# Performance work log

Measured on AMD Instinct MI355X. Metric: run time of the kernel, lower is better.

## Reference

```python
import jax, jax.numpy as jnp
import numpy as np
import math

NLAT, NLON, LMAX, MMAX = 128, 256, 50, 50
K = 3  # three_nn

# ---- precompute: Clenshaw-Curtis quadrature (torch_harmonics 'equiangular') ----
def _cc_nodes_weights(n):
    Nn = n - 1
    theta = np.pi * np.arange(n) / Nn
    v = np.zeros(n)
    for k in range(1, Nn // 2 + 1):
        b = 1.0 if 2 * k == Nn else 2.0
        v += b * np.cos(2 * k * theta) / (4 * k * k - 1)
    w = (2.0 / Nn) * (1.0 - v)
    w[0] *= 0.5
    w[-1] *= 0.5
    return np.cos(theta), w

# ---- precompute: orthonormal associated Legendre P_l^m(cos theta), csphase ----
def _legpoly(lmax, mmax, cost):
    sint = np.sqrt(np.clip(1.0 - cost ** 2, 0.0, None))
    p = np.zeros((mmax, lmax, cost.shape[0]))
    pmm = np.full(cost.shape[0], np.sqrt(1.0 / (4.0 * np.pi)))
    for m in range(mmax):
        if m > 0:
            pmm = -pmm * np.sqrt((2.0 * m + 1.0) / (2.0 * m)) * sint
        p[m, m] = pmm
        if m + 1 < lmax:
            p[m, m + 1] = np.sqrt(2.0 * m + 3.0) * cost * pmm
        for l in range(m + 2, lmax):
            a = np.sqrt((4.0 * l * l - 1.0) / (l * l - m * m))
            b = np.sqrt(((2.0 * l + 1.0) * (l - 1 + m) * (l - 1 - m)) / ((2.0 * l - 3.0) * (l * l - m * m)))
            p[m, l] = a * cost * p[m, l - 1] - b * p[m, l - 2]
    return p

_cost, _w = _cc_nodes_weights(NLAT)
_PCTW = jnp.asarray((_legpoly(LMAX, MMAX, _cost) * _w[None, None, :]).astype(np.float32))  # (mmax,lmax,nlat)

_gx, _gy = np.meshgrid(np.arange(NLAT), np.arange(-NLAT, NLAT), indexing='ij')
_GRID = jnp.asarray((np.stack([_gx.ravel(), _gy.ravel()], -1) / NLAT * np.pi).astype(np.float32))  # (M,2)

_RECTW = jnp.asarray(np.exp(-(LMAX - np.arange(1, LMAX + 1)) ** 2 / (2.0 * LMAX ** 2)).astype(np.float32))  # (lmax,)


def to_spherical(coords):
    # coords: (B,N,3) -> r:(B,N), sph:(B,N,2) = [arccos(x/r), azimuth in [0,2pi)]
    sq = coords ** 2
    pn = jnp.sqrt(jnp.flip(jnp.cumsum(jnp.flip(sq, -1), -1), -1))  # pn[...,i] = ||coords[...,i:]||
    r = pn[..., 0]
    phi = jnp.arccos(coords[..., :-2] / pn[..., :-2])
    a = jnp.arccos(coords[..., -2] / pn[..., -2])
    phi_final = a + (2.0 * math.pi - 2.0 * a) * (coords[..., -1] < 0)
    return r, jnp.concatenate([phi, phi_final[..., None]], axis=-1)


def interp_to_grid(coords):
    # spherical transform + 3-NN (squared dists) + distance-weighted interpolation onto the lat/lon grid
    r, sph = to_spherical(coords)
    sph = sph.at[..., 1].add(-math.pi)
    # brute-force pairwise squared distances grid(M,2) vs sph(B,N,2): (B,M,N)
    d2 = (jnp.sum(_GRID ** 2, -1)[None, :, None] + jnp.sum(sph ** 2, -1)[:, None, :]
          - 2.0 * jnp.einsum('md,bnd->bmn', _GRID, sph))
    _, idx = jax.lax.top_k(-jax.lax.stop_gradient(d2), K)  # (B,M,K), ascending distance
    sel = jax.vmap(lambda s, i: s[i])(sph, idx)            # (B,M,K,2)
    fsel = jax.vmap(lambda f, i: f[i])(r, idx)             # (B,M,K)
    dk = jnp.sum((_GRID[None, :, None, :] - sel) ** 2, -1)  # recompute selected sq-dists (differentiable)
    w = dk / jnp.sum(dk, -1, keepdims=True)                # weights = dist / sum(dist), as in source
    return jnp.sum(fsel * w, -1).reshape(-1, NLAT, NLON)


def sht_real(x):
    # RealSHT (equiangular, ortho): rfft(norm='forward')*2pi, then Legendre*quadrature einsum; real part only
    xf = jnp.fft.rfft(x, axis=-1)[..., :MMAX] * (2.0 * math.pi / NLON)
    return jnp.einsum('bkm,mlk->blm', jnp.real(xf).astype(jnp.float32), _PCTW)  # (B,lmax,mmax)


def setup_inputs() -> dict:
    key = jax.random.key(0)
    k1, k2 = jax.random.split(key)
    pred = jax.random.normal(k1, (2, 2048, 3), dtype=jnp.float32)
    target = jax.random.normal(k2, (2, 2048, 3), dtype=jnp.float32)
    return {"pred": pred, "target": target}


def reference(pred, target):
    pc = sht_real(interp_to_grid(pred))
    tc = sht_real(interp_to_grid(target))
    return jnp.mean(jnp.sum((pc - tc) ** 2 * _RECTW[None, :, None], axis=(1, 2)))
```

## Files before the change

kernel.cpp:

```cpp
#include <hip/hip_runtime.h>
#include <math.h>

#define PI_D 3.14159265358979323846
#define PIF  3.14159265358979323846f
#define NLAT 128
#define NLON 256
#define LMAX 50
#define MMAX 50
#define NPTS 2048
#define NBT 16
#define NBA 32
#define NBIN (NBT * NBA)
#define WBIN 0.19634954084936207f
#define INVW 5.092958178940651f
#define BIG 1e30f
#define KMASK 0xFFFFF800u

__device__ __forceinline__ void insert3(float kf, float& k0, float& k1, float& k2) {
    float n1 = __builtin_amdgcn_fmed3f(kf, k0, k1);
    float n2 = __builtin_amdgcn_fmed3f(kf, k1, k2);
    k0 = fminf(kf, k0);
    k1 = n1;
    k2 = n2;
}

__device__ __forceinline__ float mkkey(float gt, float gl, float2 tl, int idx) {
    float dt = gt - tl.x, dl = gl - tl.y;
    float d = fmaf(dt, dt, dl * dl);
    return __uint_as_float((__float_as_uint(d) & KMASK) | (unsigned)idx);
}

__global__ __launch_bounds__(256) void prep_kernel(
    const float* __restrict__ pred, const float* __restrict__ tgt,
    float2* __restrict__ gbtl, float* __restrict__ gbr, int* __restrict__ goff,
    float* __restrict__ pctwT, float* __restrict__ out) {

    __shared__ float2 s_btl[NPTS];
    __shared__ float  s_br[NPTS];
    __shared__ int    s_cnt[NBIN];
    __shared__ int    s_off[NBIN + 1];

    int bid = blockIdx.x;
    int t = threadIdx.x;

    if (bid >= 4) {
        int k = bid - 4;
        int m = t;
        if (k == 0 && m == 0) out[0] = 0.0f;
        if (m >= MMAX) return;

        double thd = PI_D * (double)k / 127.0;
        float cost = (float)cos(thd);
        float sint = (float)sin(thd);

        float c2 = (float)cos(2.0 * thd);
        float two_c2 = 2.0f * c2;
        float cp = 1.0f, cc = c2, v = 0.0f;
        for (int tt = 1; tt <= 63; ++tt) {
            v += 2.0f * cc / (float)(4 * tt * tt - 1);
            float cn = two_c2 * cc - cp;
            cp = cc;
            cc = cn;
        }
        float w = (2.0f / 127.0f) * (1.0f - v);
        if (k == 0 || k == 127) w *= 0.5f;

        float pmm = sqrtf(1.0f / (4.0f * PIF));
        for (int i = 1; i <= m; ++i)
            pmm = -pmm * sqrtf((2.0f * (float)i + 1.0f) / (2.0f * (float)i)) * sint;

        float* o = pctwT + (size_t)k * MMAX + m;
        for (int l = 0; l < m; ++l) o[(size_t)l * NLAT * MMAX] = 0.0f;
        o[(size_t)m * NLAT * MMAX] = pmm * w;
        float plm2 = pmm, plm1 = 0.0f;
        if (m + 1 < LMAX) {
            plm1 = sqrtf(2.0f * (float)m + 3.0f) * cost * pmm;
            o[(size_t)(m + 1) * NLAT * MMAX] = plm1 * w;
        }
        for (int l = m + 2; l < LMAX; ++l) {
            float fl = (float)l;
            float denom = fl * fl - (float)(m * m);
            float a = sqrtf((4.0f * fl * fl - 1.0f) / denom);
            float b = sqrtf(((2.0f * fl + 1.0f) * (float)(l - 1 + m) * (float)(l - 1 - m)) /
                            ((2.0f * fl - 3.0f) * denom));
            float p = a * cost * plm1 - b * plm2;
            o[(size_t)l * NLAT * MMAX] = p * w;
            plm2 = plm1;
            plm1 = p;
        }
        return;
    }

    int f = bid;
    const float* src = ((f < 2) ? pred : tgt) + (size_t)(f & 1) * NPTS * 3;

    s_cnt[t] = 0;
    s_cnt[t + 256] = 0;
    __syncthreads();

    float pth[8], paz[8], pr[8];
    int pbin[8];
#pragma unroll
    for (int i = 0; i < 8; ++i) {
        int n = t + 256 * i;
        float x = src[3 * n], y = src[3 * n + 1], z = src[3 * n + 2];
        float s1 = z * z;
        float s2 = s1 + y * y;
        float s3 = s2 + x * x;
        float r = sqrtf(s3);
        float rho = sqrtf(s2);
        float th = acosf(x / r);
        float a = acosf(y / rho);
        float az = (z < 0.0f) ? (a + (2.0f * PIF - 2.0f * a)) : a;
        az -= PIF;
        int bt = min(max((int)(th * INVW), 0), NBT - 1);
        int ba = min(max((int)((az + PIF) * INVW), 0), NBA - 1);
        int b = bt * NBA + ba;
        pth[i] = th; paz[i] = az; pr[i] = r; pbin[i] = b;
        atomicAdd(&s_cnt[b], 1);
    }
    __syncthreads();

    if (t == 0) s_off[NBIN] = NPTS;
    if (t < 64) {
        int base = t * 8;
        int loc[8];
        int run = 0;
#pragma unroll
        for (int i = 0; i < 8; ++i) { loc[i] = run; run += s_cnt[base + i]; }
        int x = run;
#pragma unroll
        for (int d = 1; d < 64; d <<= 1) {
            int y = __shfl_up(x, d);
            if (t >= d) x += y;
        }
        int ex = x - run;
#pragma unroll
        for (int i = 0; i < 8; ++i) s_off[base + i] = ex + loc[i];
    }
    __syncthreads();
    s_cnt[t] = s_off[t];
    s_cnt[t + 256] = s_off[t + 256];
    __syncthreads();
#pragma unroll
    for (int i = 0; i < 8; ++i) {
        int pos = atomicAdd(&s_cnt[pbin[i]], 1);
        s_btl[pos] = make_float2(pth[i], paz[i]);
        s_br[pos] = pr[i];
    }
    __syncthreads();

    for (int n = t; n < NPTS; n += 256) {
        gbtl[(size_t)f * NPTS + n] = s_btl[n];
        gbr[(size_t)f * NPTS + n] = s_br[n];
    }
    for (int n = t; n <= NBIN; n += 256) goff[f * (NBIN + 1) + n] = s_off[n];
}

__global__ __launch_bounds__(256) void knn_kernel(
    const float2* __restrict__ gbtl, const float* __restrict__ gbr,
    const int* __restrict__ goff, float* __restrict__ fre) {

    __shared__ float2 s_btl[NPTS];
    __shared__ float  s_br[NPTS];
    __shared__ int    s_off[NBIN + 1];
    __shared__ float  ctab[NLON];
    __shared__ float  row[NLON];
    __shared__ float  part[200];

    int bid = blockIdx.x;
    int t = threadIdx.x;
    int f = bid >> 7;
    int lat = bid & 127;

    {
        const float4* b4 = (const float4*)(gbtl + (size_t)f * NPTS);
        float4* s4 = (float4*)s_btl;
        for (int i = t; i < NPTS / 2; i += 256) s4[i] = b4[i];
        const float4* r4 = (const float4*)(gbr + (size_t)f * NPTS);
        float4* sr4 = (float4*)s_br;
        for (int i = t; i < NPTS / 4; i += 256) sr4[i] = r4[i];
        const int* go = goff + f * (NBIN + 1);
        for (int i = t; i <= NBIN; i += 256) s_off[i] = go[i];
        ctab[t] = (float)cos(2.0 * PI_D * (double)t / (double)NLON);
    }
    __syncthreads();

    int j = t;
    float gt = (float)((double)lat * PI_D / 128.0);
    float gl = (float)(((double)j - 128.0) * PI_D / 128.0);
    float glp = gl + PIF;
    int bt0 = lat >> 3;
    int ba0 = j >> 3;

    auto scan_seg = [&](int i, int i1, float& q0, float& q1, float& q2) {
        for (; i + 4 <= i1; i += 4) {
            float2 a0 = s_btl[i];
            float2 a1 = s_btl[i + 1];
            float2 a2 = s_btl[i + 2];
            float2 a3 = s_btl[i + 3];
            insert3(mkkey(gt, gl, a0, i), q0, q1, q2);
            insert3(mkkey(gt, gl, a1, i + 1), q0, q1, q2);
            insert3(mkkey(gt, gl, a2, i + 2), q0, q1, q2);
            insert3(mkkey(gt, gl, a3, i + 3), q0, q1, q2);
        }
        for (; i < i1; ++i)
            insert3(mkkey(gt, gl, s_btl[i], i), q0, q1, q2);
    };

    float k0 = BIG, k1 = BIG, k2 = BIG;
    {
        int rtl = max(bt0 - 1, 0), rth = min(bt0 + 1, NBT - 1);
        int bal = max(ba0 - 1, 0), bah = min(ba0 + 1, NBA - 1);
        for (int bt = rtl; bt <= rth; ++bt)
            scan_seg(s_off[bt * NBA + bal], s_off[bt * NBA + bah + 1], k0, k1, k2);
    }

    bool done;
    {
        float safe = BIG;
        if (bt0 - 1 > 0)       safe = fminf(safe, gt - (float)(bt0 - 1) * WBIN);
        if (bt0 + 1 < NBT - 1) safe = fminf(safe, (float)(bt0 + 2) * WBIN - gt);
        if (ba0 - 1 > 0)       safe = fminf(safe, glp - (float)(ba0 - 1) * WBIN);
        if (ba0 + 1 < NBA - 1) safe = fminf(safe, (float)(ba0 + 2) * WBIN - glp);
        done = (k2 <= safe * safe);
    }

    for (int R = 2; R <= 31; ++R) {
        if (__all(done)) break;
        if (!done) {
            int btl = bt0 - R, bth = bt0 + R;
            int lo = max(btl, 0), hi = min(bth, NBT - 1);
            int bal = max(ba0 - R, 0), bah = min(ba0 + R, NBA - 1);
            for (int bt = lo; bt <= hi; ++bt) {
                if (bt == btl || bt == bth) {
                    scan_seg(s_off[bt * NBA + bal], s_off[bt * NBA + bah + 1], k0, k1, k2);
                } else {
                    if (ba0 - R >= 0) {
                        int b = bt * NBA + ba0 - R;
                        scan_seg(s_off[b], s_off[b + 1], k0, k1, k2);
                    }
                    if (ba0 + R <= NBA - 1) {
                        int b = bt * NBA + ba0 + R;
                        scan_seg(s_off[b], s_off[b + 1], k0, k1, k2);
                    }
                }
            }
            float safe = BIG;
            if (bt0 - R > 0)       safe = fminf(safe, gt - (float)(bt0 - R) * WBIN);
            if (bt0 + R < NBT - 1) safe = fminf(safe, (float)(bt0 + R + 1) * WBIN - gt);
            if (ba0 - R > 0)       safe = fminf(safe, glp - (float)(ba0 - R) * WBIN);
            if (ba0 + R < NBA - 1) safe = fminf(safe, (float)(ba0 + R + 1) * WBIN - glp);
            if (k2 <= safe * safe) done = true;
        }
    }

    {
        int i0 = __float_as_uint(k0) & 0x7FF;
        int i1 = __float_as_uint(k1) & 0x7FF;
        int i2 = __float_as_uint(k2) & 0x7FF;
        float2 p0 = s_btl[i0];
        float2 p1 = s_btl[i1];
        float2 p2 = s_btl[i2];
        float dt0 = gt - p0.x, dl0 = gl - p0.y;
        float dt1 = gt - p1.x, dl1 = gl - p1.y;
        float dt2 = gt - p2.x, dl2 = gl - p2.y;
        float d0 = fmaf(dt0, dt0, dl0 * dl0);
        float d1 = fmaf(dt1, dt1, dl1 * dl1);
        float d2 = fmaf(dt2, dt2, dl2 * dl2);
        float s = d0 + d1 + d2;
        row[j] = (d0 * s_br[i0] + d1 * s_br[i1] + d2 * s_br[i2]) / s;
    }
    __syncthreads();

    if (t < 200) {
        int mm = t >> 2, q = t & 3;
        int bs = q * 64;
        float a0 = 0.0f, a1 = 0.0f, a2 = 0.0f, a3 = 0.0f;
        int p = (bs * mm) & (NLON - 1);
        int st1 = mm & (NLON - 1);
        int st2 = (2 * mm) & (NLON - 1);
        int st3 = (3 * mm) & (NLON - 1);
        int st4 = (4 * mm) & (NLON - 1);
        for (int i = 0; i < 64; i += 4) {
            a0 += row[bs + i] * ctab[p];
            a1 += row[bs + i + 1] * ctab[(p + st1) & (NLON - 1)];
            a2 += row[bs + i + 2] * ctab[(p + st2) & (NLON - 1)];
            a3 += row[bs + i + 3] * ctab[(p + st3) & (NLON - 1)];
            p = (p + st4) & (NLON - 1);
        }
        part[t] = (a0 + a1) + (a2 + a3);
    }
    __syncthreads();
    if (t < MMAX) {
        const float* pp = part + t * 4;
        fre[(f * NLAT + lat) * MMAX + t] =
            ((pp[0] + pp[1]) + (pp[2] + pp[3])) * (float)(2.0 * PI_D / (double)NLON);
    }
}

__global__ __launch_bounds__(256) void contract_loss(const float* __restrict__ fre,
                                                     const float* __restrict__ pctwT,
                                                     float* __restrict__ out) {
    int b = blockIdx.x / LMAX;
    int l = blockIdx.x % LMAX;
    int mm = threadIdx.x & 63;
    int kq = threadIdx.x >> 6;
    __shared__ float sp[4][64], st_[4][64];
    float pc = 0.0f, tc = 0.0f;
    if (mm < MMAX) {
        const float* pw = pctwT + ((size_t)l * NLAT + kq * 32) * MMAX + mm;
        const float* fp = fre + ((size_t)b * NLAT + kq * 32) * MMAX + mm;
        const float* ft = fre + ((size_t)(2 + b) * NLAT + kq * 32) * MMAX + mm;
#pragma unroll 8
        for (int k = 0; k < 32; ++k) {
            float w = pw[k * MMAX];
            pc += fp[k * MMAX] * w;
            tc += ft[k * MMAX] * w;
        }
    }
    sp[kq][mm] = pc;
    st_[kq][mm] = tc;
    __syncthreads();
    if (threadIdx.x < 64) {
        int m2 = threadIdx.x;
        float pcs = (sp[0][m2] + sp[1][m2]) + (sp[2][m2] + sp[3][m2]);
        float tcs = (st_[0][m2] + st_[1][m2]) + (st_[2][m2] + st_[3][m2]);
        float diff = pcs - tcs;
        double dl_ = (double)(49 - l);
        float rw = (float)exp(-(dl_ * dl_) / 5000.0);
        float contrib = (m2 < MMAX) ? diff * diff * rw * 0.5f : 0.0f;
        for (int off = 32; off > 0; off >>= 1) contrib += __shfl_down(contrib, off);
        if (m2 == 0) atomicAdd(out, contrib);
    }
}

extern "C" void kernel_launch(void* const* d_in, const int* in_sizes, int n_in,
                              void* d_out, int out_size, void* d_ws, size_t ws_size,
                              hipStream_t stream) {
    const float* pred = (const float*)d_in[0];
    const float* tgt = (const float*)d_in[1];
    float* ws = (float*)d_ws;

    float*  pctwT = ws;
    float*  fre   = ws + 320000;
    float2* gbtl  = (float2*)(ws + 345600);
    float*  gbr   = ws + 345600 + 16384;
    int*    goff  = (int*)(ws + 345600 + 16384 + 8192);
    float* out = (float*)d_out;

    prep_kernel<<<132, 256, 0, stream>>>(pred, tgt, gbtl, gbr, goff, pctwT, out);
    knn_kernel<<<512, 256, 0, stream>>>(gbtl, gbr, goff, fre);
    contract_loss<<<2 * LMAX, 256, 0, stream>>>(fre, pctwT, out);
}
```

Baseline: 91.29 us.

## Fuse prep and kNN kernels, recomputing binned point sort per block

Merges the point-preparation kernel into the kNN/DFT kernel: each of the 512 latitude blocks now converts coordinates to spherical form and bin-sorts all 2048 points itself in shared memory, instead of reading results written to global memory by a separate launch. This removes one kernel launch, the global round-trip, and the dependency between the two kernels. In exchange the spherical conversion and counting sort are repeated 128 times per field. The DFT partial sums are also re-indexed so threads are grouped by quarter rather than interleaved.

```diff
diff --git a/kernel.cpp b/kernel.cpp
--- a/kernel.cpp
+++ b/kernel.cpp
@@ -30,21 +30,23 @@
     return __uint_as_float((__float_as_uint(d) & KMASK) | (unsigned)idx);
 }
 
-__global__ __launch_bounds__(256) void prep_kernel(
+__global__ __launch_bounds__(256) void fused_main(
     const float* __restrict__ pred, const float* __restrict__ tgt,
-    float2* __restrict__ gbtl, float* __restrict__ gbr, int* __restrict__ goff,
-    float* __restrict__ pctwT, float* __restrict__ out) {
+    float* __restrict__ pctwT, float* __restrict__ fre, float* __restrict__ out) {
 
     __shared__ float2 s_btl[NPTS];
     __shared__ float  s_br[NPTS];
     __shared__ int    s_cnt[NBIN];
     __shared__ int    s_off[NBIN + 1];
+    __shared__ float  ctab[NLON];
+    __shared__ float  row[NLON];
+    __shared__ float  part[256];
 
     int bid = blockIdx.x;
     int t = threadIdx.x;
 
-    if (bid >= 4) {
-        int k = bid - 4;
+    if (bid >= 512) {
+        int k = bid - 512;
         int m = t;
         if (k == 0 && m == 0) out[0] = 0.0f;
         if (m >= MMAX) return;
@@ -91,11 +93,13 @@
         return;
     }
 
-    int f = bid;
+    int f = bid >> 7;
+    int lat = bid & 127;
     const float* src = ((f < 2) ? pred : tgt) + (size_t)(f & 1) * NPTS * 3;
 
     s_cnt[t] = 0;
     s_cnt[t + 256] = 0;
+    ctab[t] = (float)cos(2.0 * PI_D * (double)t / (double)NLON);
     __syncthreads();
 
     float pth[8], paz[8], pr[8];
@@ -147,42 +151,6 @@
         int pos = atomicAdd(&s_cnt[pbin[i]], 1);
         s_btl[pos] = make_float2(pth[i], paz[i]);
         s_br[pos] = pr[i];
-    }
-    __syncthreads();
-
-    for (int n = t; n < NPTS; n += 256) {
-        gbtl[(size_t)f * NPTS + n] = s_btl[n];
-        gbr[(size_t)f * NPTS + n] = s_br[n];
-    }
-    for (int n = t; n <= NBIN; n += 256) goff[f * (NBIN + 1) + n] = s_off[n];
-}
-
-__global__ __launch_bounds__(256) void knn_kernel(
-    const float2* __restrict__ gbtl, const float* __restrict__ gbr,
-    const int* __restrict__ goff, float* __restrict__ fre) {
-
-    __shared__ float2 s_btl[NPTS];
-    __shared__ float  s_br[NPTS];
-    __shared__ int    s_off[NBIN + 1];
-    __shared__ float  ctab[NLON];
-    __shared__ float  row[NLON];
-    __shared__ float  part[200];
-
-    int bid = blockIdx.x;
-    int t = threadIdx.x;
-    int f = bid >> 7;
-    int lat = bid & 127;
-
-    {
-        const float4* b4 = (const float4*)(gbtl + (size_t)f * NPTS);
-        float4* s4 = (float4*)s_btl;
-        for (int i = t; i < NPTS / 2; i += 256) s4[i] = b4[i];
-        const float4* r4 = (const float4*)(gbr + (size_t)f * NPTS);
-        float4* sr4 = (float4*)s_br;
-        for (int i = t; i < NPTS / 4; i += 256) sr4[i] = r4[i];
-        const int* go = goff + f * (NBIN + 1);
-        for (int i = t; i <= NBIN; i += 256) s_off[i] = go[i];
-        ctab[t] = (float)cos(2.0 * PI_D * (double)t / (double)NLON);
     }
     __syncthreads();
 
@@ -273,29 +241,32 @@
     }
     __syncthreads();
 
-    if (t < 200) {
-        int mm = t >> 2, q = t & 3;
-        int bs = q * 64;
-        float a0 = 0.0f, a1 = 0.0f, a2 = 0.0f, a3 = 0.0f;
-        int p = (bs * mm) & (NLON - 1);
-        int st1 = mm & (NLON - 1);
-        int st2 = (2 * mm) & (NLON - 1);
-        int st3 = (3 * mm) & (NLON - 1);
-        int st4 = (4 * mm) & (NLON - 1);
-        for (int i = 0; i < 64; i += 4) {
-            a0 += row[bs + i] * ctab[p];
-            a1 += row[bs + i + 1] * ctab[(p + st1) & (NLON - 1)];
-            a2 += row[bs + i + 2] * ctab[(p + st2) & (NLON - 1)];
-            a3 += row[bs + i + 3] * ctab[(p + st3) & (NLON - 1)];
-            p = (p + st4) & (NLON - 1);
-        }
-        part[t] = (a0 + a1) + (a2 + a3);
+    {
+        int q = t >> 6;
+        int mm = t & 63;
+        if (mm < MMAX) {
+            int bs = q * 64;
+            float a0 = 0.0f, a1 = 0.0f, a2 = 0.0f, a3 = 0.0f;
+            int p = (bs * mm) & (NLON - 1);
+            int st1 = mm;
+            int st2 = (2 * mm) & (NLON - 1);
+            int st3 = (3 * mm) & (NLON - 1);
+            int st4 = (4 * mm) & (NLON - 1);
+            for (int i = 0; i < 64; i += 4) {
+                a0 += row[bs + i] * ctab[p];
+                a1 += row[bs + i + 1] * ctab[(p + st1) & (NLON - 1)];
+                a2 += row[bs + i + 2] * ctab[(p + st2) & (NLON - 1)];
+                a3 += row[bs + i + 3] * ctab[(p + st3) & (NLON - 1)];
+                p = (p + st4) & (NLON - 1);
+            }
+            part[q * 64 + mm] = (a0 + a1) + (a2 + a3);
+        }
     }
     __syncthreads();
     if (t < MMAX) {
-        const float* pp = part + t * 4;
-        fre[(f * NLAT + lat) * MMAX + t] =
-            ((pp[0] + pp[1]) + (pp[2] + pp[3])) * (float)(2.0 * PI_D / (double)NLON);
+        float v = ((part[t] + part[64 + t]) + (part[128 + t] + part[192 + t])) *
+                  (float)(2.0 * PI_D / (double)NLON);
+        fre[(f * NLAT + lat) * MMAX + t] = v;
     }
 }
 
@@ -342,14 +313,10 @@
     const float* tgt = (const float*)d_in[1];
     float* ws = (float*)d_ws;
 
-    float*  pctwT = ws;
-    float*  fre   = ws + 320000;
-    float2* gbtl  = (float2*)(ws + 345600);
-    float*  gbr   = ws + 345600 + 16384;
-    int*    goff  = (int*)(ws + 345600 + 16384 + 8192);
+    float* pctwT = ws;
+    float* fre   = ws + 320000;
     float* out = (float*)d_out;
 
-    prep_kernel<<<132, 256, 0, stream>>>(pred, tgt, gbtl, gbr, goff, pctwT, out);
-    knn_kernel<<<512, 256, 0, stream>>>(gbtl, gbr, goff, fre);
+    fused_main<<<640, 256, 0, stream>>>(pred, tgt, pctwT, fre, out);
     contract_loss<<<2 * LMAX, 256, 0, stream>>>(fre, pctwT, out);
 }
```

Result: faster. 84.11 us (-7.9%).
